# Kernel optimization log

Hardware: AMD Instinct MI355X
Metric: run time of the kernel (lower is better)

The kernel has to match this reference:

```python
import jax, jax.numpy as jnp
import numpy as np

N_NODES = 50000
N_EDGES = 800000
NUM_GRAPHS = 64
D_IN = 128
D_HID = 128
D_OUT = 1
SLOPE = 0.01  # default leaky_relu negative slope


def setup_inputs() -> dict:
    key = jax.random.key(0)
    ks = jax.random.split(key, 8)
    x = jax.random.normal(ks[0], (N_NODES, D_IN), dtype=jnp.float32)
    edge_index = jax.random.randint(ks[1], (2, N_EDGES), 0, N_NODES, dtype=jnp.int64)
    batch = jnp.sort(jax.random.randint(ks[2], (N_NODES,), 0, NUM_GRAPHS, dtype=jnp.int64))
    s_in = 1.0 / np.sqrt(D_IN)
    s_h = 1.0 / np.sqrt(D_HID)
    W0 = jax.random.uniform(ks[3], (D_IN, D_HID), jnp.float32, -s_in, s_in)
    W1 = jax.random.uniform(ks[4], (D_HID, D_HID), jnp.float32, -s_h, s_h)
    W2 = jax.random.uniform(ks[5], (D_HID, D_HID), jnp.float32, -s_h, s_h)
    Wfc1 = jax.random.uniform(ks[6], (D_HID, D_HID), jnp.float32, -s_h, s_h)
    Wfc2 = jax.random.uniform(ks[7], (D_HID, D_OUT), jnp.float32, -s_h, s_h)
    return {"x": x, "edge_index": edge_index, "batch": batch,
            "W0": W0, "W1": W1, "W2": W2, "Wfc1": Wfc1, "Wfc2": Wfc2}


def _leaky(v):
    return jnp.where(v >= 0, v, SLOPE * v)


def _gcn_layer(x, row, col, dinv, W):
    # GCNConv: h = x W; out = D^-1/2 (A+I) D^-1/2 h  (unit edge weights)
    h = x @ W
    coef = (dinv[row] * dinv[col])[:, None]            # [E,1]
    agg = jax.ops.segment_sum(h[row] * coef, col, num_segments=N_NODES)
    return agg + h * (dinv * dinv)[:, None]            # self-loop term


def reference(x, edge_index, batch, W0, W1, W2, Wfc1, Wfc2):
    row, col = edge_index[0], edge_index[1]
    # degree with self loops (edge weight 1); same for all layers
    deg = jax.ops.segment_sum(jnp.ones(N_EDGES, x.dtype), col, num_segments=N_NODES) + 1.0
    dinv = jax.lax.rsqrt(deg)
    h = x
    for W in (W0, W1, W2):
        h = _leaky(_gcn_layer(h, row, col, dinv, W))
    y = _leaky(h @ Wfc1)
    y = _leaky(y @ Wfc2)                               # [N, 1]
    # avg_pool_x(batch, y, batch): mean of y per graph id
    sums = jax.ops.segment_sum(y, batch, num_segments=NUM_GRAPHS)
    cnts = jax.ops.segment_sum(jnp.ones(N_NODES, y.dtype), batch, num_segments=NUM_GRAPHS)
    return sums / jnp.maximum(cnts, 1.0)[:, None]      # [NUM_GRAPHS, 1]
```

## Files before the change

### kernel.cpp

```cpp
#include <hip/hip_runtime.h>

#define N_NODES   50000
#define N_EDGES   800000
#define NUM_GRAPHS 64
#define D         128
#define SLOPE     0.01

typedef double d4 __attribute__((ext_vector_type(4)));

__device__ __forceinline__ double dleaky(double v) { return v >= 0.0 ? v : SLOPE * v; }

__global__ void zero_kernel(int* __restrict__ p, int n) {
    int i = blockIdx.x * blockDim.x + threadIdx.x;
    if (i < n) p[i] = 0;
}

__global__ void hist_kernel(const int* __restrict__ col, int* __restrict__ hist, int E) {
    int e = blockIdx.x * blockDim.x + threadIdx.x;
    if (e < E) atomicAdd(&hist[col[e]], 1);
}

__global__ void dinv_kernel(const int* __restrict__ hist, double* __restrict__ dinvd, int n) {
    int i = blockIdx.x * blockDim.x + threadIdx.x;
    if (i < n) dinvd[i] = 1.0 / sqrt((double)hist[i] + 1.0);
}

__global__ __launch_bounds__(256) void scan1(const int* __restrict__ hist,
                                             int* __restrict__ start,
                                             int* __restrict__ bsum, int n) {
    __shared__ int tmp[256];
    const int tid = threadIdx.x;
    int base = blockIdx.x * 1024 + tid * 4;
    int v[4]; int s = 0;
#pragma unroll
    for (int i = 0; i < 4; ++i) { int idx = base + i; v[i] = (idx < n) ? hist[idx] : 0; s += v[i]; }
    tmp[tid] = s;
    __syncthreads();
    for (int off = 1; off < 256; off <<= 1) {
        int t = (tid >= off) ? tmp[tid - off] : 0;
        __syncthreads();
        tmp[tid] += t;
        __syncthreads();
    }
    int run = tmp[tid] - s;
    if (tid == 255) bsum[blockIdx.x] = tmp[255];
#pragma unroll
    for (int i = 0; i < 4; ++i) { int idx = base + i; if (idx < n) start[idx] = run; run += v[i]; }
}

__global__ __launch_bounds__(256) void scan2(int* __restrict__ bsum, int nb,
                                             int* __restrict__ start, int n) {
    __shared__ int tmp[256];
    const int tid = threadIdx.x;
    int v = (tid < nb) ? bsum[tid] : 0;
    tmp[tid] = v;
    __syncthreads();
    for (int off = 1; off < 256; off <<= 1) {
        int t = (tid >= off) ? tmp[tid - off] : 0;
        __syncthreads();
        tmp[tid] += t;
        __syncthreads();
    }
    if (tid < nb) bsum[tid] = tmp[tid] - v;
    if (tid == 255) start[n] = tmp[255];
}

__global__ __launch_bounds__(256) void scan3(int* __restrict__ start, int* __restrict__ cursor,
                                             const int* __restrict__ bsum, int n) {
    int off = bsum[blockIdx.x];
    int base = blockIdx.x * 1024 + threadIdx.x * 4;
#pragma unroll
    for (int i = 0; i < 4; ++i) {
        int j = base + i;
        if (j < n) { int v = start[j] + off; start[j] = v; cursor[j] = v; }
    }
}

__global__ void build_kernel(const int* __restrict__ row, const int* __restrict__ col,
                             int* __restrict__ cursor, int* __restrict__ srcrow, int E) {
    int e = blockIdx.x * blockDim.x + threadIdx.x;
    if (e >= E) return;
    int p = atomicAdd(&cursor[col[e]], 1);
    srcrow[p] = row[e];
}

__global__ void gbound_kernel(const int* __restrict__ batch, int* __restrict__ gstart, int n) {
    int i = blockIdx.x * blockDim.x + threadIdx.x;
    if (i >= n) return;
    int b = batch[i];
    int prev = (i == 0) ? -1 : batch[i - 1];
    for (int g = prev + 1; g <= b; ++g) gstart[g] = i;
    if (i == n - 1) {
        for (int g = b + 1; g <= NUM_GRAPHS; ++g) gstart[g] = n;
    }
}

__global__ __launch_bounds__(256, 4) void gemm128_mfma(const float* __restrict__ A,
                                                       const float* __restrict__ W,
                                                       float* __restrict__ C, int M, int act,
                                                       const double* __restrict__ scale) {
    __shared__ double As[32][33];
    __shared__ float  Ws[32][129];
    const int tid  = threadIdx.x;
    const int lane = tid & 63;
    const int wid  = tid >> 6;
    const int wrow = wid >> 1;
    const int wcol = wid & 1;
    const int rowBase = blockIdx.x * 32;

    d4 acc0 = {0.0, 0.0, 0.0, 0.0};
    d4 acc1 = {0.0, 0.0, 0.0, 0.0};
    d4 acc2 = {0.0, 0.0, 0.0, 0.0};
    d4 acc3 = {0.0, 0.0, 0.0, 0.0};

    const int lr = tid >> 3;
    const int lc = (tid & 7) * 4;
    const int wr = tid & 31;
    const int wc = (tid >> 5) * 16;

    const int growA = rowBase + lr;
    const bool haveA = (growA < M);

    float4 a0 = make_float4(0.f, 0.f, 0.f, 0.f);
    if (haveA) a0 = *reinterpret_cast<const float4*>(A + (size_t)growA * D + lc);

    const int arow = wrow * 16 + (lane & 15);
    const int asub = lane >> 4;
    const int bcol = wcol * 64 + (lane & 15);

    for (int kc = 0; kc < 128; kc += 32) {
        As[lr][lc + 0] = (double)a0.x;
        As[lr][lc + 1] = (double)a0.y;
        As[lr][lc + 2] = (double)a0.z;
        As[lr][lc + 3] = (double)a0.w;
        {
            const float4* src = reinterpret_cast<const float4*>(W + (size_t)(kc + wr) * D + wc);
#pragma unroll
            for (int i = 0; i < 4; ++i)
                *reinterpret_cast<float4*>(&Ws[wr][wc + 4 * i]) = src[i];
        }
        __syncthreads();

        if (kc + 32 < 128 && haveA)
            a0 = *reinterpret_cast<const float4*>(A + (size_t)growA * D + (kc + 32) + lc);

#pragma unroll
        for (int kk = 0; kk < 8; ++kk) {
            double av = As[arow][kk * 4 + asub];
            double b0 = (double)Ws[kk * 4 + asub][bcol +  0];
            double b1 = (double)Ws[kk * 4 + asub][bcol + 16];
            double b2 = (double)Ws[kk * 4 + asub][bcol + 32];
            double b3 = (double)Ws[kk * 4 + asub][bcol + 48];
            acc0 = __builtin_amdgcn_mfma_f64_16x16x4f64(av, b0, acc0, 0, 0, 0);
            acc1 = __builtin_amdgcn_mfma_f64_16x16x4f64(av, b1, acc1, 0, 0, 0);
            acc2 = __builtin_amdgcn_mfma_f64_16x16x4f64(av, b2, acc2, 0, 0, 0);
            acc3 = __builtin_amdgcn_mfma_f64_16x16x4f64(av, b3, acc3, 0, 0, 0);
        }
        __syncthreads();
    }

    const int rbase = rowBase + wrow * 16 + 4 * (lane >> 4);
    const int cb = wcol * 64 + (lane & 15);
#pragma unroll
    for (int r = 0; r < 4; ++r) {
        int grow = rbase + r;
        if (grow < M) {
            double sc = scale ? scale[grow] : 1.0;
            double v0 = acc0[r], v1 = acc1[r], v2 = acc2[r], v3 = acc3[r];
            if (act) { v0 = dleaky(v0); v1 = dleaky(v1); v2 = dleaky(v2); v3 = dleaky(v3); }
            v0 *= sc; v1 *= sc; v2 *= sc; v3 *= sc;
            float* crow = C + (size_t)grow * D + cb;
            crow[ 0] = (float)v0;
            crow[16] = (float)v1;
            crow[32] = (float)v2;
            crow[48] = (float)v3;
        }
    }
}

__global__ __launch_bounds__(256) void agg_half(const float* __restrict__ hp,
                                                const int* __restrict__ srcrow,
                                                const int* __restrict__ start,
                                                const double* __restrict__ dinvd,
                                                float* __restrict__ out, int n) {
    const int bid  = blockIdx.x;
    const int fs   = bid & 1;
    const int node = (bid >> 1) * 4 + (int)(threadIdx.x >> 6);
    const int lane = threadIdx.x & 63;
    if (node >= n) return;
    int s = start[node], e = start[node + 1];
    double dn = dinvd[node];
    const int off = fs * 64 + lane;
    float hs = hp[(size_t)node * D + off];
    double ax = 0.0;
    int p = s;
    for (; p + 16 <= e; p += 16) {
        int r[16]; float hv[16];
#pragma unroll
        for (int i = 0; i < 16; ++i) r[i] = srcrow[p + i];
#pragma unroll
        for (int i = 0; i < 16; ++i) hv[i] = hp[(size_t)r[i] * D + off];
#pragma unroll
        for (int i = 0; i < 16; ++i) ax += (double)hv[i];
    }
    for (; p + 8 <= e; p += 8) {
        int r[8]; float hv[8];
#pragma unroll
        for (int i = 0; i < 8; ++i) r[i] = srcrow[p + i];
#pragma unroll
        for (int i = 0; i < 8; ++i) hv[i] = hp[(size_t)r[i] * D + off];
#pragma unroll
        for (int i = 0; i < 8; ++i) ax += (double)hv[i];
    }
    for (; p < e; ++p) {
        int r = srcrow[p];
        ax += (double)hp[(size_t)r * D + off];
    }
    ax = dleaky((ax + (double)hs) * dn);
    out[(size_t)node * D + off] = (float)ax;
}

__global__ __launch_bounds__(256) void fc2_d(const float* __restrict__ y,
                                             const float* __restrict__ w,
                                             double* __restrict__ s, int n) {
    int node = (int)((blockIdx.x * blockDim.x + threadIdx.x) >> 6);
    int lane = threadIdx.x & 63;
    if (node >= n) return;
    float2 yv = *reinterpret_cast<const float2*>(y + (size_t)node * D + lane * 2);
    float2 wv = *reinterpret_cast<const float2*>(w + lane * 2);
    double part = (double)yv.x * (double)wv.x + (double)yv.y * (double)wv.y;
#pragma unroll
    for (int off = 32; off > 0; off >>= 1) part += __shfl_down(part, off, 64);
    if (lane == 0) s[node] = dleaky(part);
}

__global__ __launch_bounds__(256) void pool2(const double* __restrict__ s,
                                             const int* __restrict__ gstart,
                                             float* __restrict__ out) {
    __shared__ double lsum[256];
    const int g = blockIdx.x;
    const int tid = threadIdx.x;
    const int s0 = gstart[g], s1 = gstart[g + 1];
    double sum = 0.0;
    for (int i = s0 + tid; i < s1; i += 256) sum += s[i];
    lsum[tid] = sum;
    __syncthreads();
    for (int off = 128; off > 0; off >>= 1) {
        if (tid < off) lsum[tid] += lsum[tid + off];
        __syncthreads();
    }
    if (tid == 0) {
        int cnt = s1 - s0;
        out[g] = (float)(lsum[0] / (double)(cnt > 0 ? cnt : 1));
    }
}

extern "C" void kernel_launch(void* const* d_in, const int* in_sizes, int n_in,
                              void* d_out, int out_size, void* d_ws, size_t ws_size,
                              hipStream_t stream) {
    const float* x    = (const float*)d_in[0];
    const int*   eidx = (const int*)d_in[1];
    const int*   batch= (const int*)d_in[2];
    const float* W0   = (const float*)d_in[3];
    const float* W1   = (const float*)d_in[4];
    const float* W2   = (const float*)d_in[5];
    const float* Wfc1 = (const float*)d_in[6];
    const float* Wfc2 = (const float*)d_in[7];
    float* out = (float*)d_out;

    const int* erow = eidx;
    const int* ecol = eidx + N_EDGES;

    char* ws = (char*)d_ws;
    int*    hist   = (int*)   (ws + 0);
    int*    start  = (int*)   (ws + 200064);
    int*    cursor = (int*)   (ws + 400384);
    int*    bsum   = (int*)   (ws + 600448);
    double* dinvd  = (double*)(ws + 600704);
    int*    srcrow = (int*)   (ws + 1000704);
    double* svec   = (double*)(ws + 4200704);
    float*  bufA   = (float*) (ws + 4600832);
    float*  bufB   = (float*) (ws + 30200832);
    int*    gstart = cursor;

    zero_kernel<<<(N_NODES + 255) / 256, 256, 0, stream>>>(hist, N_NODES);
    hist_kernel<<<(N_EDGES + 255) / 256, 256, 0, stream>>>(ecol, hist, N_EDGES);
    dinv_kernel<<<(N_NODES + 255) / 256, 256, 0, stream>>>(hist, dinvd, N_NODES);

    const int NB = (N_NODES + 1023) / 1024;
    scan1<<<NB, 256, 0, stream>>>(hist, start, bsum, N_NODES);
    scan2<<<1, 256, 0, stream>>>(bsum, NB, start, N_NODES);
    scan3<<<NB, 256, 0, stream>>>(start, cursor, bsum, N_NODES);

    build_kernel<<<(N_EDGES + 255) / 256, 256, 0, stream>>>(erow, ecol, cursor, srcrow, N_EDGES);
    gbound_kernel<<<(N_NODES + 255) / 256, 256, 0, stream>>>(batch, gstart, N_NODES);

    const int GEMM_GRID = (N_NODES + 31) / 32;
    const int AGG_GRID  = 2 * ((N_NODES + 3) / 4);
    const int FC2_GRID  = (N_NODES + 3) / 4;

    gemm128_mfma<<<GEMM_GRID, 256, 0, stream>>>(x, W0, bufA, N_NODES, 0, dinvd);
    agg_half<<<AGG_GRID, 256, 0, stream>>>(bufA, srcrow, start, dinvd, bufB, N_NODES);
    gemm128_mfma<<<GEMM_GRID, 256, 0, stream>>>(bufB, W1, bufA, N_NODES, 0, dinvd);
    agg_half<<<AGG_GRID, 256, 0, stream>>>(bufA, srcrow, start, dinvd, bufB, N_NODES);
    gemm128_mfma<<<GEMM_GRID, 256, 0, stream>>>(bufB, W2, bufA, N_NODES, 0, dinvd);
    agg_half<<<AGG_GRID, 256, 0, stream>>>(bufA, srcrow, start, dinvd, bufB, N_NODES);
    gemm128_mfma<<<GEMM_GRID, 256, 0, stream>>>(bufB, Wfc1, bufA, N_NODES, 1, (const double*)nullptr);

    fc2_d<<<FC2_GRID, 256, 0, stream>>>(bufA, Wfc2, svec, N_NODES);
    pool2<<<NUM_GRAPHS, 256, 0, stream>>>(svec, gstart, out);
}
```

Measured before the change: 466.9 us.

## Split aggregation across 16-feature slices with edge-parallel lanes per wavefront

Replaces the half-feature aggregation kernel with one that splits the 128 features into 8 slices of 16. Within a wavefront, 4 groups of 16 lanes each take a different edge, and the partial sums are combined with cross-lane shuffles. The goal is more edge-level parallelism and more blocks in flight for the gather-bound step. The cost is 64-byte gather segments instead of 256-byte ones, 4x more blocks, and a redundant per-node load of start and dinv in every slice.

```diff
diff --git a/kernel.cpp b/kernel.cpp
--- a/kernel.cpp
+++ b/kernel.cpp
@@ -178,46 +178,49 @@
     }
 }
 
-__global__ __launch_bounds__(256) void agg_half(const float* __restrict__ hp,
-                                                const int* __restrict__ srcrow,
-                                                const int* __restrict__ start,
-                                                const double* __restrict__ dinvd,
-                                                float* __restrict__ out, int n) {
-    const int bid  = blockIdx.x;
-    const int fs   = bid & 1;
-    const int node = (bid >> 1) * 4 + (int)(threadIdx.x >> 6);
-    const int lane = threadIdx.x & 63;
+__global__ __launch_bounds__(256) void agg_slice(const float* __restrict__ hp,
+                                                 const int* __restrict__ srcrow,
+                                                 const int* __restrict__ start,
+                                                 const double* __restrict__ dinvd,
+                                                 float* __restrict__ out, int n) {
+    const int bid   = blockIdx.x;
+    const int slice = bid & 7;
+    const int node  = (bid >> 3) * 4 + (int)(threadIdx.x >> 6);
+    const int lane  = threadIdx.x & 63;
     if (node >= n) return;
-    int s = start[node], e = start[node + 1];
-    double dn = dinvd[node];
-    const int off = fs * 64 + lane;
-    float hs = hp[(size_t)node * D + off];
+    const int es = lane >> 4;
+    const int f  = slice * 16 + (lane & 15);
+    const int s = start[node], e = start[node + 1];
+    const double dn = dinvd[node];
+    const float hs = hp[(size_t)node * D + f];
     double ax = 0.0;
     int p = s;
     for (; p + 16 <= e; p += 16) {
-        int r[16]; float hv[16];
-#pragma unroll
-        for (int i = 0; i < 16; ++i) r[i] = srcrow[p + i];
-#pragma unroll
-        for (int i = 0; i < 16; ++i) hv[i] = hp[(size_t)r[i] * D + off];
-#pragma unroll
-        for (int i = 0; i < 16; ++i) ax += (double)hv[i];
-    }
-    for (; p + 8 <= e; p += 8) {
-        int r[8]; float hv[8];
-#pragma unroll
-        for (int i = 0; i < 8; ++i) r[i] = srcrow[p + i];
-#pragma unroll
-        for (int i = 0; i < 8; ++i) hv[i] = hp[(size_t)r[i] * D + off];
-#pragma unroll
-        for (int i = 0; i < 8; ++i) ax += (double)hv[i];
-    }
-    for (; p < e; ++p) {
-        int r = srcrow[p];
-        ax += (double)hp[(size_t)r * D + off];
-    }
-    ax = dleaky((ax + (double)hs) * dn);
-    out[(size_t)node * D + off] = (float)ax;
+        int r0 = srcrow[p + es];
+        int r1 = srcrow[p + 4 + es];
+        int r2 = srcrow[p + 8 + es];
+        int r3 = srcrow[p + 12 + es];
+        float h0 = hp[(size_t)r0 * D + f];
+        float h1 = hp[(size_t)r1 * D + f];
+        float h2 = hp[(size_t)r2 * D + f];
+        float h3 = hp[(size_t)r3 * D + f];
+        ax += (double)h0; ax += (double)h1; ax += (double)h2; ax += (double)h3;
+    }
+    for (; p + 4 <= e; p += 4) {
+        int r = srcrow[p + es];
+        ax += (double)hp[(size_t)r * D + f];
+    }
+    const int rem = e - p;
+    if (es < rem) {
+        int r = srcrow[p + es];
+        ax += (double)hp[(size_t)r * D + f];
+    }
+    ax += __shfl_xor(ax, 16, 64);
+    ax += __shfl_xor(ax, 32, 64);
+    if (es == 0) {
+        double v = dleaky((ax + (double)hs) * dn);
+        out[(size_t)node * D + f] = (float)v;
+    }
 }
 
 __global__ __launch_bounds__(256) void fc2_d(const float* __restrict__ y,
@@ -296,15 +299,15 @@
     gbound_kernel<<<(N_NODES + 255) / 256, 256, 0, stream>>>(batch, gstart, N_NODES);
 
     const int GEMM_GRID = (N_NODES + 31) / 32;
-    const int AGG_GRID  = 2 * ((N_NODES + 3) / 4);
+    const int AGG_GRID  = 8 * ((N_NODES + 3) / 4);
     const int FC2_GRID  = (N_NODES + 3) / 4;
 
     gemm128_mfma<<<GEMM_GRID, 256, 0, stream>>>(x, W0, bufA, N_NODES, 0, dinvd);
-    agg_half<<<AGG_GRID, 256, 0, stream>>>(bufA, srcrow, start, dinvd, bufB, N_NODES);
+    agg_slice<<<AGG_GRID, 256, 0, stream>>>(bufA, srcrow, start, dinvd, bufB, N_NODES);
     gemm128_mfma<<<GEMM_GRID, 256, 0, stream>>>(bufB, W1, bufA, N_NODES, 0, dinvd);
-    agg_half<<<AGG_GRID, 256, 0, stream>>>(bufA, srcrow, start, dinvd, bufB, N_NODES);
+    agg_slice<<<AGG_GRID, 256, 0, stream>>>(bufA, srcrow, start, dinvd, bufB, N_NODES);
     gemm128_mfma<<<GEMM_GRID, 256, 0, stream>>>(bufB, W2, bufA, N_NODES, 0, dinvd);
-    agg_half<<<AGG_GRID, 256, 0, stream>>>(bufA, srcrow, start, dinvd, bufB, N_NODES);
+    agg_slice<<<AGG_GRID, 256, 0, stream>>>(bufA, srcrow, start, dinvd, bufB, N_NODES);
     gemm128_mfma<<<GEMM_GRID, 256, 0, stream>>>(bufB, Wfc1, bufA, N_NODES, 1, (const double*)nullptr);
 
     fc2_d<<<FC2_GRID, 256, 0, stream>>>(bufA, Wfc2, svec, N_NODES);
```

Result: slower. 705.6 us (+51.1%).
